# Kernel tuning notes

Measured on AMD Instinct MI355X. Metric: run time of the kernel, lower is better.

## Reference

```python
import jax, jax.numpy as jnp
import numpy as np

C_Z = 128
C_HIDDEN = 128
EPS = 1e-5


def _layer_norm(x, w, b):
    mu = jnp.mean(x, axis=-1, keepdims=True)
    var = jnp.var(x, axis=-1, keepdims=True)
    return (x - mu) * jax.lax.rsqrt(var + EPS) * w + b


def setup_inputs() -> dict:
    key = jax.random.key(0)
    ks = jax.random.split(key, 8)
    B, N = 1, 384
    z = jax.random.normal(ks[0], (B, N, N, C_Z), dtype=jnp.float32)
    mask = jnp.ones((B, N, N), dtype=jnp.float32)
    s_z = 1.0 / np.sqrt(C_Z)
    s_h = 1.0 / np.sqrt(C_HIDDEN)
    return {
        "z": z,
        "mask": mask,
        # projection linears (lecun-like random init)
        "w_ap": jax.random.normal(ks[1], (C_HIDDEN, C_Z), jnp.float32) * s_z,
        "b_ap": jnp.zeros((C_HIDDEN,), jnp.float32),
        "w_bp": jax.random.normal(ks[2], (C_HIDDEN, C_Z), jnp.float32) * s_z,
        "b_bp": jnp.zeros((C_HIDDEN,), jnp.float32),
        # gating linears: torch init is zeros weight / ones bias, but use small
        # random weights so gradients are non-trivial; bias = 1 as in 'gating' init
        "w_ag": jax.random.normal(ks[3], (C_HIDDEN, C_Z), jnp.float32) * s_z,
        "b_ag": jnp.ones((C_HIDDEN,), jnp.float32),
        "w_bg": jax.random.normal(ks[4], (C_HIDDEN, C_Z), jnp.float32) * s_z,
        "b_bg": jnp.ones((C_HIDDEN,), jnp.float32),
        "w_g": jax.random.normal(ks[5], (C_Z, C_Z), jnp.float32) * s_z,
        "b_g": jnp.ones((C_Z,), jnp.float32),
        # final output linear ('final' init is zeros; randomize for a useful baseline)
        "w_z": jax.random.normal(ks[6], (C_Z, C_HIDDEN), jnp.float32) * s_h,
        "b_z": jnp.zeros((C_Z,), jnp.float32),
        "ln_in_w": jnp.ones((C_Z,), jnp.float32),
        "ln_in_b": jnp.zeros((C_Z,), jnp.float32),
        "ln_out_w": jnp.ones((C_HIDDEN,), jnp.float32),
        "ln_out_b": jnp.zeros((C_HIDDEN,), jnp.float32),
    }


def reference(z, mask, w_ap, b_ap, w_bp, b_bp, w_ag, b_ag, w_bg, b_bg,
              w_g, b_g, w_z, b_z, ln_in_w, ln_in_b, ln_out_w, ln_out_b):
    # z: [B, N, N, C_z], mask: [B, N, N]
    m = mask[..., None]
    zn = _layer_norm(z, ln_in_w, ln_in_b)
    a = (zn @ w_ap.T + b_ap) * jax.nn.sigmoid(zn @ w_ag.T + b_ag) * m
    b = (zn @ w_bp.T + b_bp) * jax.nn.sigmoid(zn @ w_bg.T + b_bg) * m
    # outgoing: a -> [B,C,i,j], b -> [B,C,j,i]
    a_p = jnp.transpose(a, (0, 3, 1, 2))
    b_p = jnp.transpose(b, (0, 3, 2, 1))
    # NOTE: repo's einsum has no contracted index -> elementwise product a*b
    x = jnp.einsum('bcij,bcji->bijc', a_p, b_p)  # [B, N, N, C_hidden]
    x = _layer_norm(x, ln_out_w, ln_out_b)
    x = x @ w_z.T + b_z
    g = jax.nn.sigmoid(zn @ w_g.T + b_g)
    return x * g
```

## Files before the change

kernel.cpp:

```cpp
#include <hip/hip_runtime.h>

#define NN 384
#define CC 128
#define PP (NN*NN)
#define PB 128
#define NB (PP/PB)
#define TPB 256

typedef __attribute__((ext_vector_type(8))) short bf16x8;
typedef __attribute__((ext_vector_type(16))) float f32x16;
typedef __attribute__((ext_vector_type(8))) unsigned short u16x8;

#define ROWT(reg,h) ((((reg)&3) + 8*((reg)>>2)) + 4*(h))

__device__ __forceinline__ unsigned short f2bf(float f){
  unsigned u = __float_as_uint(f);
  u += 0x7FFFu + ((u>>16)&1u);
  return (unsigned short)(u>>16);
}
__device__ __forceinline__ float bf2f(unsigned h){ return __uint_as_float(h<<16); }
__device__ __forceinline__ unsigned pack2(float a, float b){
  return (unsigned)f2bf(a) | ((unsigned)f2bf(b)<<16);
}
__device__ __forceinline__ float sigmoidf_(float x){
  return __fdividef(1.0f, 1.0f + __expf(-x));
}

__global__ __launch_bounds__(256) void k0_wprep(
    const float* __restrict__ wap, const float* __restrict__ wag,
    const float* __restrict__ wbp, const float* __restrict__ wbg,
    const float* __restrict__ wg,  const float* __restrict__ wz,
    unsigned short* __restrict__ wfrag){
  int tid = blockIdx.x*256 + threadIdx.x;
  int plane = tid >> 11, chunk = tid & 2047;
  const float* W = (plane==0||plane==2) ? wap
                 : (plane==1||plane==3) ? wag
                 : (plane==4||plane==6) ? wbp
                 : (plane==5||plane==7) ? wbg
                 : (plane==8) ? wz : wg;
  bool lo = (plane==2)||(plane==3)||(plane==6)||(plane==7);
  int k0 = chunk >> 8, n = (chunk >> 6) & 3, l = chunk & 63;
  int o  = n*32 + (l & 31);
  int kb = k0*16 + ((l>>5)<<3);
  const float* s = W + o*128 + kb;
  u16x8 v;
  #pragma unroll
  for (int e=0;e<8;e++){
    float w = s[e];
    unsigned short hh = f2bf(w);
    v[e] = lo ? f2bf(w - bf2f(hh)) : hh;
  }
  *(u16x8*)(wfrag + (size_t)tid*8) = v;
}

__device__ __forceinline__ void stage_half(const unsigned char* __restrict__ src_base,
                                           unsigned char* slot, int t){
  int wv = t>>6, l = t&63;
  const unsigned char* src = src_base + wv*4096 + l*16;
  unsigned char* dst = slot + wv*4096;
  #pragma unroll
  for (int i=0;i<4;i++)
    __builtin_amdgcn_global_load_lds(
        (const __attribute__((address_space(1))) unsigned int*)(src + i*1024),
        (__attribute__((address_space(3))) unsigned int*)(dst + i*1024),
        16, 0, 0);
}

__device__ __forceinline__ void pass_H16(const bf16x8* a, int kbase,
    const unsigned char* slot, int l, f32x16* acc){
  #pragma unroll
  for (int kr=0;kr<4;kr++){
    #pragma unroll
    for (int n=0;n<4;n++){
      bf16x8 f = *(const bf16x8*)(slot + (kr*4+n)*1024 + l*16);
      acc[n] = __builtin_amdgcn_mfma_f32_32x32x16_bf16(a[kbase+kr], f, acc[n],0,0,0);
    }
  }
}
__device__ __forceinline__ void pass_HL16(const bf16x8* aH, const bf16x8* aL, int kbase,
    const unsigned char* slot, int l, f32x16* acc){
  #pragma unroll
  for (int kr=0;kr<4;kr++){
    #pragma unroll
    for (int n=0;n<4;n++){
      bf16x8 f = *(const bf16x8*)(slot + (kr*4+n)*1024 + l*16);
      acc[n] = __builtin_amdgcn_mfma_f32_32x32x16_bf16(aH[kbase+kr], f, acc[n],0,0,0);
      acc[n] = __builtin_amdgcn_mfma_f32_32x32x16_bf16(aL[kbase+kr], f, acc[n],0,0,0);
    }
  }
}
__device__ __forceinline__ void splat(const float* __restrict__ b, int c, f32x16* acc){
  #pragma unroll
  for (int n=0;n<4;n++){
    float v = b[n*32+c];
    #pragma unroll
    for (int r=0;r<16;r++) acc[n][r]=v;
  }
}
__device__ __forceinline__ void extract8(const unsigned char* R0, int row, int h,
                                         bf16x8 a[8]){
  int swz = (row&7)<<4;
  #pragma unroll
  for (int k0=0;k0<8;k0++){
    unsigned off = (unsigned)(row*256 + (((k0<<5) + (h<<4)) ^ swz));
    a[k0] = *(const bf16x8*)(R0 + off);
  }
}

__global__ __launch_bounds__(TPB,2) void k_fused(
    const float* __restrict__ z, const float* __restrict__ mask,
    const float* __restrict__ bap, const float* __restrict__ bag,
    const float* __restrict__ bbp, const float* __restrict__ bbg,
    const float* __restrict__ bgg, const float* __restrict__ bz,
    const float* __restrict__ lniw, const float* __restrict__ lnib,
    const float* __restrict__ lnow, const float* __restrict__ lnob,
    const unsigned short* __restrict__ wfrag,
    float* __restrict__ out){
  __shared__ unsigned char lds[65536];
  unsigned char* R0 = lds;
  const unsigned char* wfrag8 = (const unsigned char*)wfrag;
  const int t = threadIdx.x;
  const int pos0 = blockIdx.x * PB;
  const int rowg = t>>5, c4 = (t&31)<<2;

  stage_half(wfrag8, lds + 32768, t);

  float4 nv[16];
  {
    float4 lw = *(const float4*)(lniw + c4);
    float4 lb = *(const float4*)(lnib + c4);
    #pragma unroll
    for (int it=0; it<16; ++it){
      int row = it*8 + rowg;
      float4 v = *(const float4*)(z + (size_t)(pos0+row)*CC + c4);
      float s = v.x+v.y+v.z+v.w;
      #pragma unroll
      for (int mm=1; mm<32; mm<<=1) s += __shfl_xor(s,mm);
      float mu = s*(1.0f/128.0f);
      float d0=v.x-mu, d1=v.y-mu, d2=v.z-mu, d3=v.w-mu;
      float ss = d0*d0+d1*d1+d2*d2+d3*d3;
      #pragma unroll
      for (int mm=1; mm<32; mm<<=1) ss += __shfl_xor(ss,mm);
      float rstd = rsqrtf(ss*(1.0f/128.0f) + 1e-5f);
      nv[it].x = d0*rstd*lw.x+lb.x; nv[it].y = d1*rstd*lw.y+lb.y;
      nv[it].z = d2*rstd*lw.z+lb.z; nv[it].w = d3*rstd*lw.w+lb.w;
      unsigned off = (unsigned)(row*256 + ((c4<<1) ^ ((row&7)<<4)));
      *(uint2*)(R0 + off) = make_uint2(pack2(nv[it].x, nv[it].y),
                                       pack2(nv[it].z, nv[it].w));
    }
  }
  __syncthreads();

  const int wv = t>>6, l = t&63;
  const int c  = l&31, h = l>>5;
  const int row0 = wv*32;

  bf16x8 aH[8], aLo[8];
  extract8(R0, row0+c, h, aH);
  __syncthreads();
  #pragma unroll
  for (int it=0;it<16;++it){
    int row = it*8 + rowg;
    float l0 = nv[it].x - bf2f(f2bf(nv[it].x)), l1 = nv[it].y - bf2f(f2bf(nv[it].y));
    float l2 = nv[it].z - bf2f(f2bf(nv[it].z)), l3 = nv[it].w - bf2f(f2bf(nv[it].w));
    unsigned off = (unsigned)(row*256 + ((c4<<1) ^ ((row&7)<<4)));
    *(uint2*)(R0+off) = make_uint2(pack2(l0,l1), pack2(l2,l3));
  }
  __syncthreads();
  extract8(R0, row0+c, h, aLo);

  f32x16 accp[4], accg[4];
#define SL(p) (lds + 32768 + (((p)&1)<<14))
#define PH(p) do{ __syncthreads(); \
    if ((p)+1 < 20) stage_half(wfrag8 + ((size_t)((p)+1))*16384, SL((p)+1), t); }while(0)

  PH(0);  splat(bap,c,accp); pass_HL16(aH,aLo,0,SL(0), l,accp);
  PH(1);  pass_HL16(aH,aLo,4,SL(1), l,accp);
  PH(2);  splat(bag,c,accg); pass_HL16(aH,aLo,0,SL(2), l,accg);
  PH(3);  pass_HL16(aH,aLo,4,SL(3), l,accg);
  PH(4);  pass_H16(aH,0,SL(4), l,accp);
  PH(5);  pass_H16(aH,4,SL(5), l,accp);
  PH(6);  pass_H16(aH,0,SL(6), l,accg);
  PH(7);  pass_H16(aH,4,SL(7), l,accg);
  {
    unsigned char* xr = R0 + wv*8192;
    #pragma unroll
    for (int n=0;n<4;n++){
      #pragma unroll
      for (int j=0;j<8;j++){
        float m0 = mask[pos0+row0+ROWT(2*j,  h)];
        float m1 = mask[pos0+row0+ROWT(2*j+1,h)];
        float a0 = accp[n][2*j]  *sigmoidf_(accg[n][2*j])  *m0;
        float a1 = accp[n][2*j+1]*sigmoidf_(accg[n][2*j+1])*m1;
        *(unsigned*)(xr + (n*8+j)*256 + l*4) = pack2(a0,a1);
      }
    }
  }
  PH(8);  splat(bbp,c,accp); pass_HL16(aH,aLo,0,SL(8), l,accp);
  PH(9);  pass_HL16(aH,aLo,4,SL(9), l,accp);
  PH(10); splat(bbg,c,accg); pass_HL16(aH,aLo,0,SL(10),l,accg);
  PH(11); pass_HL16(aH,aLo,4,SL(11),l,accg);
  PH(12); pass_H16(aH,0,SL(12),l,accp);
  PH(13); pass_H16(aH,4,SL(13),l,accp);
  PH(14); pass_H16(aH,0,SL(14),l,accg);
  PH(15); pass_H16(aH,4,SL(15),l,accg);
  bf16x8 a2[8];
  {
    f32x16 xv[4];
    const unsigned char* xr = R0 + wv*8192;
    #pragma unroll
    for (int n=0;n<4;n++){
      #pragma unroll
      for (int j=0;j<8;j++){
        float m0 = mask[pos0+row0+ROWT(2*j,  h)];
        float m1 = mask[pos0+row0+ROWT(2*j+1,h)];
        unsigned w = *(const unsigned*)(xr + (n*8+j)*256 + l*4);
        float b0 = accp[n][2*j]  *sigmoidf_(accg[n][2*j])  *m0;
        float b1 = accp[n][2*j+1]*sigmoidf_(accg[n][2*j+1])*m1;
        xv[n][2*j]   = bf2f(w & 0xffffu)*b0;
        xv[n][2*j+1] = bf2f(w >> 16)   *b1;
      }
    }
    float lw4[4], lb4[4];
    #pragma unroll
    for (int n=0;n<4;n++){ lw4[n]=lnow[n*32+c]; lb4[n]=lnob[n*32+c]; }
    #pragma unroll
    for (int reg=0; reg<16; ++reg){
      float s=0.f;
      #pragma unroll
      for (int n=0;n<4;n++) s += xv[n][reg];
      #pragma unroll
      for (int mm=1; mm<32; mm<<=1) s += __shfl_xor(s,mm);
      float mu = s*(1.0f/128.0f);
      float ss=0.f;
      #pragma unroll
      for (int n=0;n<4;n++){ float d=xv[n][reg]-mu; ss+=d*d; }
      #pragma unroll
      for (int mm=1; mm<32; mm<<=1) ss += __shfl_xor(ss,mm);
      float rstd = rsqrtf(ss*(1.0f/128.0f)+1e-5f);
      int row = row0 + ROWT(reg,h);
      int swz = (row&7)<<4;
      #pragma unroll
      for (int n=0;n<4;n++){
        int colb = (n*32+c)*2;
        float vvv = (xv[n][reg]-mu)*rstd*lw4[n]+lb4[n];
        *(unsigned short*)(R0 + row*256 + (colb ^ swz)) = f2bf(vvv);
      }
    }
    extract8(R0, row0+c, h, a2);
  }
  PH(16); splat(bz,c,accp);  pass_H16(a2,0,SL(16),l,accp);
  PH(17); pass_H16(a2,4,SL(17),l,accp);
  PH(18); splat(bgg,c,accg); pass_H16(aH,0,SL(18),l,accg);
  PH(19); pass_H16(aH,4,SL(19),l,accg);
  #pragma unroll
  for (int n=0;n<4;n++){
    #pragma unroll
    for (int reg=0; reg<16; ++reg){
      int row = row0 + ROWT(reg,h);
      out[(size_t)(pos0+row)*CC + n*32 + c] = accp[n][reg]*sigmoidf_(accg[n][reg]);
    }
  }
#undef PH
#undef SL
}

extern "C" void kernel_launch(void* const* d_in, const int* in_sizes, int n_in,
                              void* d_out, int out_size, void* d_ws, size_t ws_size,
                              hipStream_t stream){
  const float* z     = (const float*)d_in[0];
  const float* mask  = (const float*)d_in[1];
  const float* w_ap  = (const float*)d_in[2];
  const float* b_ap  = (const float*)d_in[3];
  const float* w_bp  = (const float*)d_in[4];
  const float* b_bp  = (const float*)d_in[5];
  const float* w_ag  = (const float*)d_in[6];
  const float* b_ag  = (const float*)d_in[7];
  const float* w_bg  = (const float*)d_in[8];
  const float* b_bg  = (const float*)d_in[9];
  const float* w_g   = (const float*)d_in[10];
  const float* b_g   = (const float*)d_in[11];
  const float* w_z   = (const float*)d_in[12];
  const float* b_z   = (const float*)d_in[13];
  const float* ln_in_w  = (const float*)d_in[14];
  const float* ln_in_b  = (const float*)d_in[15];
  const float* ln_out_w = (const float*)d_in[16];
  const float* ln_out_b = (const float*)d_in[17];

  unsigned short* wfrag = (unsigned short*)d_ws;

  k0_wprep<<<80, 256, 0, stream>>>(w_ap, w_ag, w_bp, w_bg, w_g, w_z, wfrag);
  k_fused<<<NB, TPB, 0, stream>>>(z, mask, b_ap, b_ag, b_bp, b_bg, b_g, b_z,
                                  ln_in_w, ln_in_b, ln_out_w, ln_out_b,
                                  wfrag, (float*)d_out);
}
```

Measured before the change: 127.0 us.

## Halve weight staging slots to shrink LDS and raise occupancy to 3 blocks

Weight fragments are now streamed in 8 KB quarter-K chunks over 40 double-buffered phases instead of 16 KB chunks over 20. This cuts the kernel's LDS from 64 KB to 48 KB so three blocks can fit per CU, and launch bounds are raised to 3 to match. The cost is twice as many barriers and smaller load batches per phase, plus tighter register limits that could cause spills. The manual bf16 rounding is also replaced with the HIP library conversion.

```diff
diff --git a/kernel.cpp b/kernel.cpp
--- a/kernel.cpp
+++ b/kernel.cpp
@@ -1,4 +1,5 @@
 #include <hip/hip_runtime.h>
+#include <hip/hip_bf16.h>
 
 #define NN 384
 #define CC 128
@@ -14,9 +15,8 @@
 #define ROWT(reg,h) ((((reg)&3) + 8*((reg)>>2)) + 4*(h))
 
 __device__ __forceinline__ unsigned short f2bf(float f){
-  unsigned u = __float_as_uint(f);
-  u += 0x7FFFu + ((u>>16)&1u);
-  return (unsigned short)(u>>16);
+  __hip_bfloat16 h = __float2bfloat16(f);
+  return __builtin_bit_cast(unsigned short, h);
 }
 __device__ __forceinline__ float bf2f(unsigned h){ return __uint_as_float(h<<16); }
 __device__ __forceinline__ unsigned pack2(float a, float b){
@@ -53,23 +53,23 @@
   *(u16x8*)(wfrag + (size_t)tid*8) = v;
 }
 
-__device__ __forceinline__ void stage_half(const unsigned char* __restrict__ src_base,
-                                           unsigned char* slot, int t){
+__device__ __forceinline__ void stage_q(const unsigned char* __restrict__ src_base,
+                                        unsigned char* slot, int t){
   int wv = t>>6, l = t&63;
-  const unsigned char* src = src_base + wv*4096 + l*16;
-  unsigned char* dst = slot + wv*4096;
-  #pragma unroll
-  for (int i=0;i<4;i++)
+  const unsigned char* src = src_base + wv*2048 + l*16;
+  unsigned char* dst = slot + wv*2048;
+  #pragma unroll
+  for (int i=0;i<2;i++)
     __builtin_amdgcn_global_load_lds(
         (const __attribute__((address_space(1))) unsigned int*)(src + i*1024),
         (__attribute__((address_space(3))) unsigned int*)(dst + i*1024),
         16, 0, 0);
 }
 
-__device__ __forceinline__ void pass_H16(const bf16x8* a, int kbase,
+__device__ __forceinline__ void q_H(const bf16x8* a, int kbase,
     const unsigned char* slot, int l, f32x16* acc){
   #pragma unroll
-  for (int kr=0;kr<4;kr++){
+  for (int kr=0;kr<2;kr++){
     #pragma unroll
     for (int n=0;n<4;n++){
       bf16x8 f = *(const bf16x8*)(slot + (kr*4+n)*1024 + l*16);
@@ -77,10 +77,10 @@
     }
   }
 }
-__device__ __forceinline__ void pass_HL16(const bf16x8* aH, const bf16x8* aL, int kbase,
+__device__ __forceinline__ void q_HL(const bf16x8* aH, const bf16x8* aL, int kbase,
     const unsigned char* slot, int l, f32x16* acc){
   #pragma unroll
-  for (int kr=0;kr<4;kr++){
+  for (int kr=0;kr<2;kr++){
     #pragma unroll
     for (int n=0;n<4;n++){
       bf16x8 f = *(const bf16x8*)(slot + (kr*4+n)*1024 + l*16);
@@ -107,7 +107,7 @@
   }
 }
 
-__global__ __launch_bounds__(TPB,2) void k_fused(
+__global__ __launch_bounds__(TPB,3) void k_fused(
     const float* __restrict__ z, const float* __restrict__ mask,
     const float* __restrict__ bap, const float* __restrict__ bag,
     const float* __restrict__ bbp, const float* __restrict__ bbg,
@@ -116,14 +116,14 @@
     const float* __restrict__ lnow, const float* __restrict__ lnob,
     const unsigned short* __restrict__ wfrag,
     float* __restrict__ out){
-  __shared__ unsigned char lds[65536];
+  __shared__ unsigned char lds[49152];
   unsigned char* R0 = lds;
   const unsigned char* wfrag8 = (const unsigned char*)wfrag;
   const int t = threadIdx.x;
   const int pos0 = blockIdx.x * PB;
   const int rowg = t>>5, c4 = (t&31)<<2;
 
-  stage_half(wfrag8, lds + 32768, t);
+  stage_q(wfrag8, lds + 32768, t);
 
   float4 nv[16];
   {
@@ -170,18 +170,26 @@
   extract8(R0, row0+c, h, aLo);
 
   f32x16 accp[4], accg[4];
-#define SL(p) (lds + 32768 + (((p)&1)<<14))
+#define SL(p) (lds + 32768 + (((p)&1)<<13))
 #define PH(p) do{ __syncthreads(); \
-    if ((p)+1 < 20) stage_half(wfrag8 + ((size_t)((p)+1))*16384, SL((p)+1), t); }while(0)
-
-  PH(0);  splat(bap,c,accp); pass_HL16(aH,aLo,0,SL(0), l,accp);
-  PH(1);  pass_HL16(aH,aLo,4,SL(1), l,accp);
-  PH(2);  splat(bag,c,accg); pass_HL16(aH,aLo,0,SL(2), l,accg);
-  PH(3);  pass_HL16(aH,aLo,4,SL(3), l,accg);
-  PH(4);  pass_H16(aH,0,SL(4), l,accp);
-  PH(5);  pass_H16(aH,4,SL(5), l,accp);
-  PH(6);  pass_H16(aH,0,SL(6), l,accg);
-  PH(7);  pass_H16(aH,4,SL(7), l,accg);
+    if ((p)+1 < 40) stage_q(wfrag8 + ((size_t)((p)+1))*8192, SL((p)+1), t); }while(0)
+
+  PH(0);  splat(bap,c,accp); q_HL(aH,aLo,0,SL(0), l,accp);
+  PH(1);  q_HL(aH,aLo,2,SL(1), l,accp);
+  PH(2);  q_HL(aH,aLo,4,SL(2), l,accp);
+  PH(3);  q_HL(aH,aLo,6,SL(3), l,accp);
+  PH(4);  splat(bag,c,accg); q_HL(aH,aLo,0,SL(4), l,accg);
+  PH(5);  q_HL(aH,aLo,2,SL(5), l,accg);
+  PH(6);  q_HL(aH,aLo,4,SL(6), l,accg);
+  PH(7);  q_HL(aH,aLo,6,SL(7), l,accg);
+  PH(8);  q_H(aH,0,SL(8), l,accp);
+  PH(9);  q_H(aH,2,SL(9), l,accp);
+  PH(10); q_H(aH,4,SL(10),l,accp);
+  PH(11); q_H(aH,6,SL(11),l,accp);
+  PH(12); q_H(aH,0,SL(12),l,accg);
+  PH(13); q_H(aH,2,SL(13),l,accg);
+  PH(14); q_H(aH,4,SL(14),l,accg);
+  PH(15); q_H(aH,6,SL(15),l,accg);
   {
     unsigned char* xr = R0 + wv*8192;
     #pragma unroll
@@ -196,14 +204,22 @@
       }
     }
   }
-  PH(8);  splat(bbp,c,accp); pass_HL16(aH,aLo,0,SL(8), l,accp);
-  PH(9);  pass_HL16(aH,aLo,4,SL(9), l,accp);
-  PH(10); splat(bbg,c,accg); pass_HL16(aH,aLo,0,SL(10),l,accg);
-  PH(11); pass_HL16(aH,aLo,4,SL(11),l,accg);
-  PH(12); pass_H16(aH,0,SL(12),l,accp);
-  PH(13); pass_H16(aH,4,SL(13),l,accp);
-  PH(14); pass_H16(aH,0,SL(14),l,accg);
-  PH(15); pass_H16(aH,4,SL(15),l,accg);
+  PH(16); splat(bbp,c,accp); q_HL(aH,aLo,0,SL(16),l,accp);
+  PH(17); q_HL(aH,aLo,2,SL(17),l,accp);
+  PH(18); q_HL(aH,aLo,4,SL(18),l,accp);
+  PH(19); q_HL(aH,aLo,6,SL(19),l,accp);
+  PH(20); splat(bbg,c,accg); q_HL(aH,aLo,0,SL(20),l,accg);
+  PH(21); q_HL(aH,aLo,2,SL(21),l,accg);
+  PH(22); q_HL(aH,aLo,4,SL(22),l,accg);
+  PH(23); q_HL(aH,aLo,6,SL(23),l,accg);
+  PH(24); q_H(aH,0,SL(24),l,accp);
+  PH(25); q_H(aH,2,SL(25),l,accp);
+  PH(26); q_H(aH,4,SL(26),l,accp);
+  PH(27); q_H(aH,6,SL(27),l,accp);
+  PH(28); q_H(aH,0,SL(28),l,accg);
+  PH(29); q_H(aH,2,SL(29),l,accg);
+  PH(30); q_H(aH,4,SL(30),l,accg);
+  PH(31); q_H(aH,6,SL(31),l,accg);
   bf16x8 a2[8];
   {
     f32x16 xv[4];
@@ -249,10 +265,14 @@
     }
     extract8(R0, row0+c, h, a2);
   }
-  PH(16); splat(bz,c,accp);  pass_H16(a2,0,SL(16),l,accp);
-  PH(17); pass_H16(a2,4,SL(17),l,accp);
-  PH(18); splat(bgg,c,accg); pass_H16(aH,0,SL(18),l,accg);
-  PH(19); pass_H16(aH,4,SL(19),l,accg);
+  PH(32); splat(bz,c,accp);  q_H(a2,0,SL(32),l,accp);
+  PH(33); q_H(a2,2,SL(33),l,accp);
+  PH(34); q_H(a2,4,SL(34),l,accp);
+  PH(35); q_H(a2,6,SL(35),l,accp);
+  PH(36); splat(bgg,c,accg); q_H(aH,0,SL(36),l,accg);
+  PH(37); q_H(aH,2,SL(37),l,accg);
+  PH(38); q_H(aH,4,SL(38),l,accg);
+  PH(39); q_H(aH,6,SL(39),l,accg);
   #pragma unroll
   for (int n=0;n<4;n++){
     #pragma unroll
```

Measured after the change: 279.5 us. 120% more time.

## Compute gates in single bf16, store sigmoid as fp16 to halve accumulators

Applied to the files above, without the earlier changes.

Gate projections now use only the high bf16 part of the input instead of hi+lo split MFMAs, which cuts weight planes from 20 to 16 and removes a chunk of MFMA work. Each gate is computed first and its sigmoid is packed into fp16 registers, so one set of accumulators serves both the gate and the projection, lowering register pressure. The layer-norm row mapping is changed so each wave owns its rows, which removes several block-wide barriers around the hi/lo staging. Mask values are hoisted into registers. In exchange, gate precision drops to single bf16 input and the sigmoid is stored in fp16.

```diff
diff --git a/kernel.cpp b/kernel.cpp
--- a/kernel.cpp
+++ b/kernel.cpp
@@ -1,4 +1,6 @@
 #include <hip/hip_runtime.h>
+#include <hip/hip_bf16.h>
+#include <hip/hip_fp16.h>
 
 #define NN 384
 #define CC 128
@@ -13,10 +15,10 @@
 
 #define ROWT(reg,h) ((((reg)&3) + 8*((reg)>>2)) + 4*(h))
 
+
 __device__ __forceinline__ unsigned short f2bf(float f){
-  unsigned u = __float_as_uint(f);
-  u += 0x7FFFu + ((u>>16)&1u);
-  return (unsigned short)(u>>16);
+  __hip_bfloat16 h = __float2bfloat16(f);
+  return __builtin_bit_cast(unsigned short, h);
 }
 __device__ __forceinline__ float bf2f(unsigned h){ return __uint_as_float(h<<16); }
 __device__ __forceinline__ unsigned pack2(float a, float b){
@@ -24,6 +26,17 @@
 }
 __device__ __forceinline__ float sigmoidf_(float x){
   return __fdividef(1.0f, 1.0f + __expf(-x));
+}
+__device__ __forceinline__ unsigned short f2h(float f){
+  __half h = __float2half(f);
+  return __builtin_bit_cast(unsigned short, h);
+}
+__device__ __forceinline__ float h2f(unsigned short u){
+  __half h = __builtin_bit_cast(__half, u);
+  return __half2float(h);
+}
+__device__ __forceinline__ unsigned pack2h(float a, float b){
+  return (unsigned)f2h(a) | ((unsigned)f2h(b)<<16);
 }
 
 __global__ __launch_bounds__(256) void k0_wprep(
@@ -33,12 +46,12 @@
     unsigned short* __restrict__ wfrag){
   int tid = blockIdx.x*256 + threadIdx.x;
   int plane = tid >> 11, chunk = tid & 2047;
-  const float* W = (plane==0||plane==2) ? wap
-                 : (plane==1||plane==3) ? wag
-                 : (plane==4||plane==6) ? wbp
-                 : (plane==5||plane==7) ? wbg
-                 : (plane==8) ? wz : wg;
-  bool lo = (plane==2)||(plane==3)||(plane==6)||(plane==7);
+  const float* W = (plane==0) ? wag
+                 : (plane==1||plane==2) ? wap
+                 : (plane==3) ? wbg
+                 : (plane==4||plane==5) ? wbp
+                 : (plane==6) ? wg : wz;
+  bool lo = (plane==2)||(plane==5);
   int k0 = chunk >> 8, n = (chunk >> 6) & 3, l = chunk & 63;
   int o  = n*32 + (l & 31);
   int kb = k0*16 + ((l>>5)<<3);
@@ -66,7 +79,7 @@
         16, 0, 0);
 }
 
-__device__ __forceinline__ void pass_H16(const bf16x8* a, int kbase,
+__device__ __forceinline__ void pass_H(const bf16x8* a, int kbase,
     const unsigned char* slot, int l, f32x16* acc){
   #pragma unroll
   for (int kr=0;kr<4;kr++){
@@ -77,7 +90,7 @@
     }
   }
 }
-__device__ __forceinline__ void pass_HL16(const bf16x8* aH, const bf16x8* aL, int kbase,
+__device__ __forceinline__ void pass_HL(const bf16x8* aH, const bf16x8* aL, int kbase,
     const unsigned char* slot, int l, f32x16* acc){
   #pragma unroll
   for (int kr=0;kr<4;kr++){
@@ -89,7 +102,8 @@
     }
   }
 }
-__device__ __forceinline__ void splat(const float* __restrict__ b, int c, f32x16* acc){
+__device__ __forceinline__ void bias_init32(const float* __restrict__ b, int c,
+                                            f32x16* acc){
   #pragma unroll
   for (int n=0;n<4;n++){
     float v = b[n*32+c];
@@ -117,21 +131,24 @@
     const unsigned short* __restrict__ wfrag,
     float* __restrict__ out){
   __shared__ unsigned char lds[65536];
-  unsigned char* R0 = lds;
+  unsigned char* buf = lds;
   const unsigned char* wfrag8 = (const unsigned char*)wfrag;
   const int t = threadIdx.x;
   const int pos0 = blockIdx.x * PB;
-  const int rowg = t>>5, c4 = (t&31)<<2;
+  const int wv = t>>6, l = t&63;
+  const int h = l>>5, c = l&31;
+  const int c4 = c<<2;
+  const int row0 = wv*32;
 
   stage_half(wfrag8, lds + 32768, t);
 
-  float4 nv[16];
+  unsigned plr[32];
   {
     float4 lw = *(const float4*)(lniw + c4);
     float4 lb = *(const float4*)(lnib + c4);
     #pragma unroll
     for (int it=0; it<16; ++it){
-      int row = it*8 + rowg;
+      int row = row0 + it*2 + h;
       float4 v = *(const float4*)(z + (size_t)(pos0+row)*CC + c4);
       float s = v.x+v.y+v.z+v.w;
       #pragma unroll
@@ -142,81 +159,85 @@
       #pragma unroll
       for (int mm=1; mm<32; mm<<=1) ss += __shfl_xor(ss,mm);
       float rstd = rsqrtf(ss*(1.0f/128.0f) + 1e-5f);
-      nv[it].x = d0*rstd*lw.x+lb.x; nv[it].y = d1*rstd*lw.y+lb.y;
-      nv[it].z = d2*rstd*lw.z+lb.z; nv[it].w = d3*rstd*lw.w+lb.w;
+      float n0=d0*rstd*lw.x+lb.x, n1=d1*rstd*lw.y+lb.y;
+      float n2=d2*rstd*lw.z+lb.z, n3=d3*rstd*lw.w+lb.w;
+      unsigned short hh0=f2bf(n0), hh1=f2bf(n1), hh2=f2bf(n2), hh3=f2bf(n3);
       unsigned off = (unsigned)(row*256 + ((c4<<1) ^ ((row&7)<<4)));
-      *(uint2*)(R0 + off) = make_uint2(pack2(nv[it].x, nv[it].y),
-                                       pack2(nv[it].z, nv[it].w));
-    }
-  }
-  __syncthreads();
-
-  const int wv = t>>6, l = t&63;
-  const int c  = l&31, h = l>>5;
-  const int row0 = wv*32;
-
+      *(uint2*)(buf + off) = make_uint2((unsigned)hh0|((unsigned)hh1<<16),
+                                        (unsigned)hh2|((unsigned)hh3<<16));
+      plr[it*2]   = pack2(n0-bf2f(hh0), n1-bf2f(hh1));
+      plr[it*2+1] = pack2(n2-bf2f(hh2), n3-bf2f(hh3));
+    }
+  }
   bf16x8 aH[8], aLo[8];
-  extract8(R0, row0+c, h, aH);
-  __syncthreads();
-  #pragma unroll
-  for (int it=0;it<16;++it){
-    int row = it*8 + rowg;
-    float l0 = nv[it].x - bf2f(f2bf(nv[it].x)), l1 = nv[it].y - bf2f(f2bf(nv[it].y));
-    float l2 = nv[it].z - bf2f(f2bf(nv[it].z)), l3 = nv[it].w - bf2f(f2bf(nv[it].w));
+  extract8(buf, row0+c, h, aH);
+  #pragma unroll
+  for (int it=0; it<16; ++it){
+    int row = row0 + it*2 + h;
     unsigned off = (unsigned)(row*256 + ((c4<<1) ^ ((row&7)<<4)));
-    *(uint2*)(R0+off) = make_uint2(pack2(l0,l1), pack2(l2,l3));
-  }
-  __syncthreads();
-  extract8(R0, row0+c, h, aLo);
-
-  f32x16 accp[4], accg[4];
+    *(uint2*)(buf + off) = make_uint2(plr[it*2], plr[it*2+1]);
+  }
+  extract8(buf, row0+c, h, aLo);
+
+  float mkr[16];
+  #pragma unroll
+  for (int reg=0;reg<16;reg++) mkr[reg] = mask[pos0 + row0 + ROWT(reg,h)];
+
+  f32x16 acc[4];
+  unsigned gpk[32];
+
 #define SL(p) (lds + 32768 + (((p)&1)<<14))
 #define PH(p) do{ __syncthreads(); \
-    if ((p)+1 < 20) stage_half(wfrag8 + ((size_t)((p)+1))*16384, SL((p)+1), t); }while(0)
-
-  PH(0);  splat(bap,c,accp); pass_HL16(aH,aLo,0,SL(0), l,accp);
-  PH(1);  pass_HL16(aH,aLo,4,SL(1), l,accp);
-  PH(2);  splat(bag,c,accg); pass_HL16(aH,aLo,0,SL(2), l,accg);
-  PH(3);  pass_HL16(aH,aLo,4,SL(3), l,accg);
-  PH(4);  pass_H16(aH,0,SL(4), l,accp);
-  PH(5);  pass_H16(aH,4,SL(5), l,accp);
-  PH(6);  pass_H16(aH,0,SL(6), l,accg);
-  PH(7);  pass_H16(aH,4,SL(7), l,accg);
+    if ((p)+1 < 16) stage_half(wfrag8 + (((size_t)((p)+1))<<14), SL((p)+1), t); }while(0)
+#define PACK_GATE() do{ \
+    _Pragma("unroll") \
+    for (int n=0;n<4;n++) \
+      _Pragma("unroll") \
+      for (int rp=0;rp<8;rp++) \
+        gpk[n*8+rp] = pack2h(sigmoidf_(acc[n][2*rp]), sigmoidf_(acc[n][2*rp+1])); \
+  }while(0)
+
+  PH(0);  bias_init32(bag,c,acc); pass_H(aH,0,SL(0), l,acc);
+  PH(1);  pass_H(aH,4,SL(1), l,acc);
+  PACK_GATE();
+  PH(2);  bias_init32(bap,c,acc); pass_HL(aH,aLo,0,SL(2), l,acc);
+  PH(3);  pass_HL(aH,aLo,4,SL(3), l,acc);
+  PH(4);  pass_H(aH,0,SL(4), l,acc);
+  PH(5);  pass_H(aH,4,SL(5), l,acc);
   {
-    unsigned char* xr = R0 + wv*8192;
+    unsigned char* xr = buf + wv*8192;
     #pragma unroll
     for (int n=0;n<4;n++){
       #pragma unroll
       for (int j=0;j<8;j++){
-        float m0 = mask[pos0+row0+ROWT(2*j,  h)];
-        float m1 = mask[pos0+row0+ROWT(2*j+1,h)];
-        float a0 = accp[n][2*j]  *sigmoidf_(accg[n][2*j])  *m0;
-        float a1 = accp[n][2*j+1]*sigmoidf_(accg[n][2*j+1])*m1;
+        float g0 = h2f((unsigned short)(gpk[n*8+j] & 0xffffu));
+        float g1 = h2f((unsigned short)(gpk[n*8+j] >> 16));
+        float a0 = acc[n][2*j]  *g0*mkr[2*j];
+        float a1 = acc[n][2*j+1]*g1*mkr[2*j+1];
         *(unsigned*)(xr + (n*8+j)*256 + l*4) = pack2(a0,a1);
       }
     }
   }
-  PH(8);  splat(bbp,c,accp); pass_HL16(aH,aLo,0,SL(8), l,accp);
-  PH(9);  pass_HL16(aH,aLo,4,SL(9), l,accp);
-  PH(10); splat(bbg,c,accg); pass_HL16(aH,aLo,0,SL(10),l,accg);
-  PH(11); pass_HL16(aH,aLo,4,SL(11),l,accg);
-  PH(12); pass_H16(aH,0,SL(12),l,accp);
-  PH(13); pass_H16(aH,4,SL(13),l,accp);
-  PH(14); pass_H16(aH,0,SL(14),l,accg);
-  PH(15); pass_H16(aH,4,SL(15),l,accg);
+  PH(6);  bias_init32(bbg,c,acc); pass_H(aH,0,SL(6), l,acc);
+  PH(7);  pass_H(aH,4,SL(7), l,acc);
+  PACK_GATE();
+  PH(8);  bias_init32(bbp,c,acc); pass_HL(aH,aLo,0,SL(8), l,acc);
+  PH(9);  pass_HL(aH,aLo,4,SL(9), l,acc);
+  PH(10); pass_H(aH,0,SL(10),l,acc);
+  PH(11); pass_H(aH,4,SL(11),l,acc);
   bf16x8 a2[8];
   {
     f32x16 xv[4];
-    const unsigned char* xr = R0 + wv*8192;
+    const unsigned char* xr = buf + wv*8192;
     #pragma unroll
     for (int n=0;n<4;n++){
       #pragma unroll
       for (int j=0;j<8;j++){
-        float m0 = mask[pos0+row0+ROWT(2*j,  h)];
-        float m1 = mask[pos0+row0+ROWT(2*j+1,h)];
+        float g0 = h2f((unsigned short)(gpk[n*8+j] & 0xffffu));
+        float g1 = h2f((unsigned short)(gpk[n*8+j] >> 16));
         unsigned w = *(const unsigned*)(xr + (n*8+j)*256 + l*4);
-        float b0 = accp[n][2*j]  *sigmoidf_(accg[n][2*j])  *m0;
-        float b1 = accp[n][2*j+1]*sigmoidf_(accg[n][2*j+1])*m1;
+        float b0 = acc[n][2*j]  *g0*mkr[2*j];
+        float b1 = acc[n][2*j+1]*g1*mkr[2*j+1];
         xv[n][2*j]   = bf2f(w & 0xffffu)*b0;
         xv[n][2*j+1] = bf2f(w >> 16)   *b1;
       }
@@ -244,25 +265,28 @@
       for (int n=0;n<4;n++){
         int colb = (n*32+c)*2;
         float vvv = (xv[n][reg]-mu)*rstd*lw4[n]+lb4[n];
-        *(unsigned short*)(R0 + row*256 + (colb ^ swz)) = f2bf(vvv);
+        *(unsigned short*)(buf + row*256 + (colb ^ swz)) = f2bf(vvv);
       }
     }
-    extract8(R0, row0+c, h, a2);
-  }
-  PH(16); splat(bz,c,accp);  pass_H16(a2,0,SL(16),l,accp);
-  PH(17); pass_H16(a2,4,SL(17),l,accp);
-  PH(18); splat(bgg,c,accg); pass_H16(aH,0,SL(18),l,accg);
-  PH(19); pass_H16(aH,4,SL(19),l,accg);
+    extract8(buf, row0+c, h, a2);
+  }
+  PH(12); bias_init32(bgg,c,acc); pass_H(aH,0,SL(12),l,acc);
+  PH(13); pass_H(aH,4,SL(13),l,acc);
+  PACK_GATE();
+  PH(14); bias_init32(bz,c,acc); pass_H(a2,0,SL(14),l,acc);
+  PH(15); pass_H(a2,4,SL(15),l,acc);
   #pragma unroll
   for (int n=0;n<4;n++){
     #pragma unroll
     for (int reg=0; reg<16; ++reg){
       int row = row0 + ROWT(reg,h);
-      out[(size_t)(pos0+row)*CC + n*32 + c] = accp[n][reg]*sigmoidf_(accg[n][reg]);
+      float gg = h2f((unsigned short)((gpk[n*8+(reg>>1)] >> ((reg&1)*16)) & 0xffffu));
+      out[(size_t)(pos0+row)*CC + n*32 + c] = acc[n][reg]*gg;
     }
   }
 #undef PH
 #undef SL
+#undef PACK_GATE
 }
 
 extern "C" void kernel_launch(void* const* d_in, const int* in_sizes, int n_in,
@@ -289,7 +313,7 @@
 
   unsigned short* wfrag = (unsigned short*)d_ws;
 
-  k0_wprep<<<80, 256, 0, stream>>>(w_ap, w_ag, w_bp, w_bg, w_g, w_z, wfrag);
+  k0_wprep<<<64, 256, 0, stream>>>(w_ap, w_ag, w_bp, w_bg, w_g, w_z, wfrag);
   k_fused<<<NB, TPB, 0, stream>>>(z, mask, b_ap, b_ag, b_bp, b_bg, b_g, b_z,
                                   ln_in_w, ln_in_b, ln_out_w, ln_out_b,
                                   wfrag, (float*)d_out);
```

Result: faster. 115.0 us (-9.5%).
